# Kernel tuning notes

Hardware: AMD Instinct MI355X
Metric: run time of the kernel (lower is better)

The kernel has to match this reference:

```python
import jax, jax.numpy as jnp
import numpy as np

B, C, H, W = 4, 64, 64, 64  # prompt and kv share the same BCHW shape
EPS = 1e-5
OFR = 4.0  # offset_range_factor
SCALE = (C // 1) ** -0.5  # n_head_channels = dim / n_heads = 64


def conv1x1(x, w, b=None):
    y = jnp.einsum('oc,bchw->bohw', w, x)
    if b is not None:
        y = y + b[None, :, None, None]
    return y


def grid_sample_bilinear(img, grid):
    # img: [N,C,Hp,Wp], grid: [N,Hg,Wg,2] with (x,y) in [-1,1], align_corners=True, zeros padding
    N, Cc, Hp, Wp = img.shape
    Hg, Wg = grid.shape[1], grid.shape[2]
    gx = (grid[..., 0] + 1.0) * 0.5 * (Wp - 1)
    gy = (grid[..., 1] + 1.0) * 0.5 * (Hp - 1)
    x0 = jnp.floor(gx)
    y0 = jnp.floor(gy)
    img_f = img.reshape(N, Cc, Hp * Wp)

    def gather(xi, yi):
        valid = (xi >= 0) & (xi <= Wp - 1) & (yi >= 0) & (yi <= Hp - 1)
        xi_c = jnp.clip(xi, 0, Wp - 1).astype(jnp.int32)
        yi_c = jnp.clip(yi, 0, Hp - 1).astype(jnp.int32)
        idx = (yi_c * Wp + xi_c).reshape(N, 1, -1)
        vals = jnp.take_along_axis(img_f, idx, axis=2)  # [N,C,Hg*Wg]
        return vals, valid.reshape(N, 1, -1).astype(img.dtype)

    v00, m00 = gather(x0, y0)
    v01, m01 = gather(x0 + 1, y0)
    v10, m10 = gather(x0, y0 + 1)
    v11, m11 = gather(x0 + 1, y0 + 1)
    wx = (gx - x0).reshape(N, 1, -1)
    wy = (gy - y0).reshape(N, 1, -1)
    out = (v00 * m00 * (1 - wx) * (1 - wy) + v01 * m01 * wx * (1 - wy)
           + v10 * m10 * (1 - wx) * wy + v11 * m11 * wx * wy)
    return out.reshape(N, Cc, Hg, Wg)


def setup_inputs() -> dict:
    key = jax.random.key(0)
    ks = jax.random.split(key, 8)
    s = 0.02
    return {
        'prompt': jax.random.normal(ks[0], (B, C, H, W), jnp.float32),
        'kv': jax.random.normal(ks[1], (B, C, H, W), jnp.float32),
        'wq': s * jax.random.normal(ks[2], (C, C), jnp.float32),
        'bq': jnp.zeros((C,), jnp.float32),
        'wk': s * jax.random.normal(ks[3], (C, C), jnp.float32),
        'bk': jnp.zeros((C,), jnp.float32),
        'wv': s * jax.random.normal(ks[4], (C, C), jnp.float32),
        'bv': jnp.zeros((C,), jnp.float32),
        'wo': s * jax.random.normal(ks[5], (C, C), jnp.float32),
        'bo': jnp.zeros((C,), jnp.float32),
        'dw_w': s * jax.random.normal(ks[6], (C, 1, 3, 3), jnp.float32),  # depthwise 3x3
        'dw_b': jnp.zeros((C,), jnp.float32),
        'ln_w': jnp.ones((C,), jnp.float32),
        'ln_b': jnp.zeros((C,), jnp.float32),
        'off_w': s * jax.random.normal(ks[7], (2, C), jnp.float32),  # 1x1 conv to 2 offset channels
    }


def reference(prompt, kv, wq, bq, wk, bk, wv, bv, wo, bo, dw_w, dw_b, ln_w, ln_b, off_w):
    # q projection (n_groups=1 so group view == full view)
    q = conv1x1(prompt, wq, bq)  # [B,C,H,W]

    # conv_offset: depthwise 3x3 -> WithBias LayerNorm over channels -> GELU -> 1x1 to 2ch
    t = jax.lax.conv_general_dilated(q, dw_w, (1, 1), ((1, 1), (1, 1)),
                                     feature_group_count=C)
    t = t + dw_b[None, :, None, None]
    mu = t.mean(axis=1, keepdims=True)
    var = t.var(axis=1, keepdims=True)
    t = (t - mu) / jnp.sqrt(var + EPS) * ln_w[None, :, None, None] + ln_b[None, :, None, None]
    t = jax.nn.gelu(t, approximate=False)
    offset = jnp.einsum('oc,bchw->bohw', off_w, t)  # [B,2,H,W] (y,x) channels

    Hk, Wk = offset.shape[2], offset.shape[3]
    n = Hk * Wk
    rng = jnp.array([1.0 / (Hk - 1.0), 1.0 / (Wk - 1.0)], dtype=offset.dtype).reshape(1, 2, 1, 1)
    offset = jnp.tanh(offset) * rng * OFR
    offset = jnp.transpose(offset, (0, 2, 3, 1))  # [B,Hk,Wk,2] (y,x)

    ref_y = (jnp.linspace(0.5, Hk - 0.5, Hk) / (Hk - 1.0)) * 2.0 - 1.0
    ref_x = (jnp.linspace(0.5, Wk - 0.5, Wk) / (Wk - 1.0)) * 2.0 - 1.0
    ry, rx = jnp.meshgrid(ref_y, ref_x, indexing='ij')
    ref = jnp.stack((ry, rx), axis=-1)[None].astype(offset.dtype)  # [1,Hk,Wk,2]

    pos = offset + ref
    grid = pos[..., ::-1]  # swap to (x,y)
    xs = grid_sample_bilinear(kv, grid)  # [B,C,Hk,Wk]
    xs = xs.reshape(B, C, n)

    k = jnp.einsum('oc,bcn->bon', wk, xs) + bk[None, :, None]
    v = jnp.einsum('oc,bcn->bon', wv, xs) + bv[None, :, None]
    qf = q.reshape(B, C, H * W)

    attn = jnp.einsum('bcm,bcn->bmn', qf, k) * SCALE  # [B,HW,n]
    attn = jax.nn.softmax(attn, axis=2)
    out = jnp.einsum('bmn,bcn->bcm', attn, v).reshape(B, C, H, W)
    return conv1x1(out, wo, bo)
```

## Files before the change

### kernel.cpp

```cpp
#include <hip/hip_runtime.h>
#include <math.h>

#define BB 4
#define CC 64
#define HH 64
#define WW 64
#define HWP 4096
#define NPTS 4096
#define NSPLIT 2
#define LDP 72
constexpr float K_EPS   = 1e-5f;
constexpr float K_SCALE = 0.125f;
constexpr float K_OFR   = 4.0f;

#define QF_OFF  0
#define QB_OFF  1048576
#define GXY_OFF 1572864
#define KB_OFF  1605632
#define VB_OFF  2129920
#define OP_OFF  2654208
#define DP_OFF  4751360

typedef short frag8 __attribute__((ext_vector_type(8)));
typedef float f32x4 __attribute__((ext_vector_type(4)));

static __device__ inline unsigned short f2bf(float f) {
  unsigned int u = __builtin_bit_cast(unsigned int, f);
  unsigned int r = (u + 0x7fffu + ((u >> 16) & 1u)) >> 16;
  return (unsigned short)r;
}

__global__ __launch_bounds__(256) void k_qproj(
    const float* __restrict__ prompt, const float* __restrict__ wq,
    const float* __restrict__ bq, float* __restrict__ qf,
    unsigned short* __restrict__ qb) {
  __shared__ float w_s[64 * 64];
  __shared__ float p_s[64 * 64];
  __shared__ unsigned short t_s[64 * 68];
  int tid = threadIdx.x;
  int blk = blockIdx.x;
  int b = blk >> 6; int hw0 = (blk & 63) * 64;
#pragma unroll
  for (int i = 0; i < 16; ++i) w_s[i * 256 + tid] = wq[i * 256 + tid];
#pragma unroll
  for (int i = 0; i < 16; ++i) {
    int idx = i * 256 + tid; int c = idx >> 6, pix = idx & 63;
    p_s[idx] = prompt[(size_t)(b * CC + c) * HWP + hw0 + pix];
  }
  __syncthreads();
  int x = tid & 63, og = tid >> 6;
  float acc[16];
#pragma unroll
  for (int oo = 0; oo < 16; ++oo) acc[oo] = bq[og * 16 + oo];
  for (int cg = 0; cg < 16; ++cg) {
    float p0 = p_s[(cg * 4 + 0) * 64 + x];
    float p1 = p_s[(cg * 4 + 1) * 64 + x];
    float p2 = p_s[(cg * 4 + 2) * 64 + x];
    float p3 = p_s[(cg * 4 + 3) * 64 + x];
#pragma unroll
    for (int oo = 0; oo < 16; ++oo) {
      const float4 w4 = *(const float4*)&w_s[(og * 16 + oo) * 64 + cg * 4];
      acc[oo] = fmaf(w4.x, p0, fmaf(w4.y, p1, fmaf(w4.z, p2, fmaf(w4.w, p3, acc[oo]))));
    }
  }
#pragma unroll
  for (int oo = 0; oo < 16; ++oo) {
    int o = og * 16 + oo;
    qf[(size_t)(b * CC + o) * HWP + hw0 + x] = acc[oo];
    t_s[x * 68 + o] = f2bf(acc[oo]);
  }
  __syncthreads();
#pragma unroll
  for (int i = 0; i < 4; ++i) {
    int idx = i * 256 + tid;
    int pix = idx >> 4, c4 = idx & 15;
    ushort4 v = *(const ushort4*)&t_s[pix * 68 + c4 * 4];
    *(ushort4*)&qb[(size_t)(b * HWP + hw0 + pix) * CC + c4 * 4] = v;
  }
}

__global__ __launch_bounds__(256) void k_offsets(
    const float* __restrict__ q, const float* __restrict__ dw_w,
    const float* __restrict__ dw_b, const float* __restrict__ ln_w,
    const float* __restrict__ ln_b, const float* __restrict__ off_w,
    float* __restrict__ gxy) {
  int tid = threadIdx.x;
  int x = tid & 63;
  int cg = tid >> 6;
  int by = blockIdx.x;
  int b = by >> 6;
  int y = by & 63;

  __shared__ float red0[4][64];
  __shared__ float red1[4][64];

  float t[16];
#pragma unroll
  for (int i = 0; i < 16; ++i) {
    int c = cg * 16 + i;
    float acc = dw_b[c];
    const float* qc = q + (size_t)(b * CC + c) * HWP;
#pragma unroll
    for (int ky = 0; ky < 3; ++ky) {
      int yy = y + ky - 1;
      bool yok = (yy >= 0) && (yy < HH);
#pragma unroll
      for (int kx = 0; kx < 3; ++kx) {
        int xx = x + kx - 1;
        bool ok = yok && (xx >= 0) && (xx < WW);
        float v = ok ? qc[yy * WW + xx] : 0.f;
        acc = fmaf(dw_w[c * 9 + ky * 3 + kx], v, acc);
      }
    }
    t[i] = acc;
  }
  float s1 = 0.f, s2 = 0.f;
#pragma unroll
  for (int i = 0; i < 16; ++i) { s1 += t[i]; s2 += t[i] * t[i]; }
  red0[cg][x] = s1;
  red1[cg][x] = s2;
  __syncthreads();
  float mu = (red0[0][x] + red0[1][x] + red0[2][x] + red0[3][x]) * (1.f / 64.f);
  float ms = (red1[0][x] + red1[1][x] + red1[2][x] + red1[3][x]) * (1.f / 64.f);
  float rstd = rsqrtf(ms - mu * mu + K_EPS);

  float oy = 0.f, ox = 0.f;
#pragma unroll
  for (int i = 0; i < 16; ++i) {
    int c = cg * 16 + i;
    float g = (t[i] - mu) * rstd * ln_w[c] + ln_b[c];
    g = 0.5f * g * (1.f + erff(g * 0.70710678118654752f));
    oy = fmaf(off_w[c], g, oy);
    ox = fmaf(off_w[CC + c], g, ox);
  }
  __syncthreads();
  red0[cg][x] = oy;
  red1[cg][x] = ox;
  __syncthreads();
  if (cg == 0) {
    float osy = red0[0][x] + red0[1][x] + red0[2][x] + red0[3][x];
    float osx = red1[0][x] + red1[1][x] + red1[2][x] + red1[3][x];
    osy = tanhf(osy) * (K_OFR / (HH - 1));
    osx = tanhf(osx) * (K_OFR / (WW - 1));
    float ry = (y + 0.5f) * (2.f / 63.f) - 1.f;
    float rx = (x + 0.5f) * (2.f / 63.f) - 1.f;
    float gx = (osx + rx + 1.f) * 0.5f * (WW - 1);
    float gy = (osy + ry + 1.f) * 0.5f * (HH - 1);
    int n = y * WW + x;
    gxy[(b * HWP + n) * 2 + 0] = gx;
    gxy[(b * HWP + n) * 2 + 1] = gy;
  }
}

__global__ __launch_bounds__(256) void k_sample_kv(
    const float* __restrict__ kv, const float* __restrict__ gxy,
    const float* __restrict__ wk, const float* __restrict__ bk,
    const float* __restrict__ wv, const float* __restrict__ bv,
    unsigned short* __restrict__ kb, unsigned short* __restrict__ vb) {
  __shared__ float wk_s[64 * 64];
  __shared__ float wv_s[64 * 64];
  __shared__ float xs_s[64 * 64];
  int tid = threadIdx.x;
  int blk = blockIdx.x;
  int b = blk >> 6; int n0 = (blk & 63) * 64;
#pragma unroll
  for (int i = 0; i < 16; ++i) {
    wk_s[i * 256 + tid] = wk[i * 256 + tid];
    wv_s[i * 256 + tid] = wv[i * 256 + tid];
  }
  int n = tid & 63, og = tid >> 6;
  int p = b * HWP + n0 + n;
  float gx = gxy[p * 2 + 0], gy = gxy[p * 2 + 1];
  float x0f = floorf(gx), y0f = floorf(gy);
  float wx = gx - x0f, wy = gy - y0f;
  int x0 = (int)x0f, y0 = (int)y0f;
  int x1 = x0 + 1, y1 = y0 + 1;
  float m00 = (x0 >= 0 && x0 < WW && y0 >= 0 && y0 < HH) ? 1.f : 0.f;
  float m01 = (x1 >= 0 && x1 < WW && y0 >= 0 && y0 < HH) ? 1.f : 0.f;
  float m10 = (x0 >= 0 && x0 < WW && y1 >= 0 && y1 < HH) ? 1.f : 0.f;
  float m11 = (x1 >= 0 && x1 < WW && y1 >= 0 && y1 < HH) ? 1.f : 0.f;
  int x0c = min(max(x0, 0), WW - 1), x1c = min(max(x1, 0), WW - 1);
  int y0c = min(max(y0, 0), HH - 1), y1c = min(max(y1, 0), HH - 1);
  int i00 = y0c * WW + x0c, i01 = y0c * WW + x1c;
  int i10 = y1c * WW + x0c, i11 = y1c * WW + x1c;
  float w00 = m00 * (1.f - wx) * (1.f - wy);
  float w01 = m01 * wx * (1.f - wy);
  float w10 = m10 * (1.f - wx) * wy;
  float w11 = m11 * wx * wy;

  const float* base = kv + (size_t)b * CC * HWP;
#pragma unroll 4
  for (int i = 0; i < 16; ++i) {
    int c = og * 16 + i;
    const float* pc = base + (size_t)c * HWP;
    xs_s[c * 64 + n] = w00 * pc[i00] + w01 * pc[i01] + w10 * pc[i10] + w11 * pc[i11];
  }
  __syncthreads();
  float ak[16], av[16];
#pragma unroll
  for (int oo = 0; oo < 16; ++oo) { ak[oo] = bk[og * 16 + oo]; av[oo] = bv[og * 16 + oo]; }
  for (int cg = 0; cg < 16; ++cg) {
    float p0 = xs_s[(cg * 4 + 0) * 64 + n];
    float p1 = xs_s[(cg * 4 + 1) * 64 + n];
    float p2 = xs_s[(cg * 4 + 2) * 64 + n];
    float p3 = xs_s[(cg * 4 + 3) * 64 + n];
#pragma unroll
    for (int oo = 0; oo < 16; ++oo) {
      int o = og * 16 + oo;
      const float4 k4 = *(const float4*)&wk_s[o * 64 + cg * 4];
      const float4 v4 = *(const float4*)&wv_s[o * 64 + cg * 4];
      ak[oo] = fmaf(k4.x, p0, fmaf(k4.y, p1, fmaf(k4.z, p2, fmaf(k4.w, p3, ak[oo]))));
      av[oo] = fmaf(v4.x, p0, fmaf(v4.y, p1, fmaf(v4.z, p2, fmaf(v4.w, p3, av[oo]))));
    }
  }
  unsigned short tk[16];
#pragma unroll
  for (int oo = 0; oo < 16; ++oo) tk[oo] = f2bf(ak[oo]);
  size_t krow = (size_t)(b * NPTS + n0 + n) * CC + og * 16;
  *(uint4*)&kb[krow]     = *(const uint4*)&tk[0];
  *(uint4*)&kb[krow + 8] = *(const uint4*)&tk[8];
#pragma unroll
  for (int oo = 0; oo < 16; ++oo) {
    int o = og * 16 + oo;
    vb[(size_t)(b * CC + o) * NPTS + n0 + n] = f2bf(av[oo]);
  }
}

__global__ __launch_bounds__(256) void k_attn(
    const unsigned short* __restrict__ qb, const unsigned short* __restrict__ kb,
    const unsigned short* __restrict__ vb, float* __restrict__ opart,
    float* __restrict__ dpart) {
  __shared__ short q_s[64 * LDP];
  __shared__ short k_s[64 * LDP];
  __shared__ short v_s[64 * LDP];
  __shared__ short p_s[64 * LDP];

  int tid = threadIdx.x;
  int w = tid >> 6, lane = tid & 63, quad = lane >> 4, l16 = lane & 15;
  int blk = blockIdx.x;
  int mt = blk & 63; int bns = blk >> 6; int ns = bns & 1; int b = bns >> 1;
  int m0 = mt * 64;

  const unsigned short* qbb = qb + (size_t)b * HWP * CC;
  const unsigned short* kbb = kb + (size_t)b * NPTS * CC;
  const unsigned short* vbb = vb + (size_t)b * CC * NPTS;

#pragma unroll
  for (int pass = 0; pass < 2; ++pass) {
    int idx = pass * 256 + tid;
    int row = idx >> 3, part = idx & 7;
    uint4 d = *(const uint4*)(qbb + (size_t)(m0 + row) * CC + part * 8);
    *(uint4*)&q_s[row * LDP + part * 8] = d;
  }

  f32x4 o_acc[4];
  float d_acc[4];
#pragma unroll
  for (int i = 0; i < 4; ++i) {
    d_acc[i] = 0.f;
    o_acc[i][0] = 0.f; o_acc[i][1] = 0.f; o_acc[i][2] = 0.f; o_acc[i][3] = 0.f;
  }

  int nbase = ns * (NPTS / NSPLIT);
  for (int it = 0; it < (NPTS / NSPLIT) / 64; ++it) {
    int n0 = nbase + it * 64;
    __syncthreads();
#pragma unroll
    for (int pass = 0; pass < 2; ++pass) {
      int idx = pass * 256 + tid;
      int row = idx >> 3, part = idx & 7;
      uint4 dk = *(const uint4*)(kbb + (size_t)(n0 + row) * CC + part * 8);
      uint4 dv = *(const uint4*)(vbb + (size_t)row * NPTS + n0 + part * 8);
      *(uint4*)&k_s[row * LDP + part * 8] = dk;
      *(uint4*)&v_s[row * LDP + part * 8] = dv;
    }
    __syncthreads();

    f32x4 s_acc[4];
#pragma unroll
    for (int t = 0; t < 4; ++t) {
      s_acc[t][0] = 0.f; s_acc[t][1] = 0.f; s_acc[t][2] = 0.f; s_acc[t][3] = 0.f;
    }
#pragma unroll
    for (int kc = 0; kc < 2; ++kc) {
      frag8 a = *(const frag8*)&q_s[(w * 16 + l16) * LDP + kc * 32 + quad * 8];
#pragma unroll
      for (int t = 0; t < 4; ++t) {
        frag8 bf = *(const frag8*)&k_s[(t * 16 + l16) * LDP + kc * 32 + quad * 8];
        s_acc[t] = __builtin_amdgcn_mfma_f32_16x16x32_bf16(a, bf, s_acc[t], 0, 0, 0);
      }
    }
#pragma unroll
    for (int t = 0; t < 4; ++t) {
#pragma unroll
      for (int r = 0; r < 4; ++r) {
        float pv = __expf(s_acc[t][r] * K_SCALE);
        unsigned short ph = f2bf(pv);
        p_s[(w * 16 + quad * 4 + r) * LDP + t * 16 + l16] = (short)ph;
        d_acc[r] += __builtin_bit_cast(float, (unsigned int)ph << 16);
      }
    }
#pragma unroll
    for (int kc = 0; kc < 2; ++kc) {
      frag8 bp = *(const frag8*)&p_s[(w * 16 + l16) * LDP + kc * 32 + quad * 8];
#pragma unroll
      for (int ct = 0; ct < 4; ++ct) {
        frag8 av = *(const frag8*)&v_s[(ct * 16 + l16) * LDP + kc * 32 + quad * 8];
        o_acc[ct] = __builtin_amdgcn_mfma_f32_16x16x32_bf16(av, bp, o_acc[ct], 0, 0, 0);
      }
    }
  }

  float* op = opart + (size_t)(ns * BB + b) * HWP * CC + (size_t)(m0 + w * 16 + l16) * CC;
#pragma unroll
  for (int ct = 0; ct < 4; ++ct) {
    float4 o4;
    o4.x = o_acc[ct][0]; o4.y = o_acc[ct][1]; o4.z = o_acc[ct][2]; o4.w = o_acc[ct][3];
    *(float4*)&op[ct * 16 + quad * 4] = o4;
  }
#pragma unroll
  for (int r = 0; r < 4; ++r) {
    float d = d_acc[r];
    d += __shfl_xor(d, 1); d += __shfl_xor(d, 2);
    d += __shfl_xor(d, 4); d += __shfl_xor(d, 8);
    if (l16 == 0)
      dpart[(ns * BB + b) * HWP + m0 + w * 16 + quad * 4 + r] = d;
  }
}

__global__ __launch_bounds__(256) void k_out(
    const float* __restrict__ opart, const float* __restrict__ dpart,
    const float* __restrict__ wo, const float* __restrict__ bo,
    float* __restrict__ out) {
  __shared__ float wo_s[CC * CC];
  __shared__ float t_s[64 * 65];
  int tid = threadIdx.x;
  int blk = blockIdx.x;
  int b = blk >> 6, mt = blk & 63, m0 = mt * 64;
  for (int i = tid; i < CC * CC; i += 256) wo_s[i] = wo[i];

  const float* o0 = opart + (size_t)(0 * BB + b) * HWP * CC;
  const float* o1 = opart + (size_t)(1 * BB + b) * HWP * CC;
  const float* d0 = dpart + (0 * BB + b) * HWP;
  const float* d1 = dpart + (1 * BB + b) * HWP;
#pragma unroll
  for (int it = 0; it < 16; ++it) {
    int idx = it * 256 + tid;
    int m = idx >> 6, c = idx & 63;
    float denom = d0[m0 + m] + d1[m0 + m];
    float val = (o0[(size_t)(m0 + m) * CC + c] + o1[(size_t)(m0 + m) * CC + c]) / denom;
    t_s[m * 65 + c] = val;
  }
  __syncthreads();
  int ml = tid & 63, og = tid >> 6;
  for (int oo = 0; oo < 16; ++oo) {
    int o = og * 16 + oo;
    float acc = bo[o];
#pragma unroll
    for (int c = 0; c < 64; ++c) acc = fmaf(wo_s[o * CC + c], t_s[ml * 65 + c], acc);
    out[(size_t)(b * CC + o) * HWP + m0 + ml] = acc;
  }
}

extern "C" void kernel_launch(void* const* d_in, const int* in_sizes, int n_in,
                              void* d_out, int out_size, void* d_ws, size_t ws_size,
                              hipStream_t stream) {
  const float* prompt = (const float*)d_in[0];
  const float* kv     = (const float*)d_in[1];
  const float* wq     = (const float*)d_in[2];
  const float* bq     = (const float*)d_in[3];
  const float* wk     = (const float*)d_in[4];
  const float* bk     = (const float*)d_in[5];
  const float* wv     = (const float*)d_in[6];
  const float* bv     = (const float*)d_in[7];
  const float* wo     = (const float*)d_in[8];
  const float* bo     = (const float*)d_in[9];
  const float* dw_w   = (const float*)d_in[10];
  const float* dw_b   = (const float*)d_in[11];
  const float* ln_w   = (const float*)d_in[12];
  const float* ln_b   = (const float*)d_in[13];
  const float* off_w  = (const float*)d_in[14];
  float* out = (float*)d_out;
  float* ws  = (float*)d_ws;

  float* qf             = ws + QF_OFF;
  unsigned short* qb    = (unsigned short*)(ws + QB_OFF);
  float* gxy            = ws + GXY_OFF;
  unsigned short* kb    = (unsigned short*)(ws + KB_OFF);
  unsigned short* vb    = (unsigned short*)(ws + VB_OFF);
  float* opart          = ws + OP_OFF;
  float* dpart          = ws + DP_OFF;

  hipLaunchKernelGGL(k_qproj, dim3(BB * 64), dim3(256), 0, stream,
                     prompt, wq, bq, qf, qb);
  hipLaunchKernelGGL(k_offsets, dim3(BB * HH), dim3(256), 0, stream,
                     qf, dw_w, dw_b, ln_w, ln_b, off_w, gxy);
  hipLaunchKernelGGL(k_sample_kv, dim3(BB * 64), dim3(256), 0, stream,
                     kv, gxy, wk, bk, wv, bv, kb, vb);
  hipLaunchKernelGGL(k_attn, dim3(BB * NSPLIT * 64), dim3(256), 0, stream,
                     qb, kb, vb, opart, dpart);
  hipLaunchKernelGGL(k_out, dim3(BB * 64), dim3(256), 0, stream,
                     opart, dpart, wo, bo, out);
}
```

Baseline: 182.5 us.

## Split attention over four key chunks with atomic accumulation and widen prep kernels

Attention blocks now split the key dimension into four chunks instead of two. Partial outputs and denominators are accumulated with atomics into one buffer that is zeroed by a memset, so k_out reads a single partial. The softmax scale is folded into the bf16 Q, Q fragments are held in registers, and the Q and P shared buffers are merged. The projection, offset and sampling kernels run 512 threads with half the per-thread work. More atomic traffic and an extra memset are traded for more blocks and a smaller reduction in the output kernel.

```diff
diff --git a/kernel.cpp b/kernel.cpp
--- a/kernel.cpp
+++ b/kernel.cpp
@@ -7,10 +7,9 @@
 #define WW 64
 #define HWP 4096
 #define NPTS 4096
-#define NSPLIT 2
+#define NSPLIT 4
 #define LDP 72
 constexpr float K_EPS   = 1e-5f;
-constexpr float K_SCALE = 0.125f;
 constexpr float K_OFR   = 4.0f;
 
 #define QF_OFF  0
@@ -19,7 +18,7 @@
 #define KB_OFF  1605632
 #define VB_OFF  2129920
 #define OP_OFF  2654208
-#define DP_OFF  4751360
+#define DP_OFF  3702784
 
 typedef short frag8 __attribute__((ext_vector_type(8)));
 typedef float f32x4 __attribute__((ext_vector_type(4)));
@@ -30,7 +29,7 @@
   return (unsigned short)r;
 }
 
-__global__ __launch_bounds__(256) void k_qproj(
+__global__ __launch_bounds__(512) void k_qproj(
     const float* __restrict__ prompt, const float* __restrict__ wq,
     const float* __restrict__ bq, float* __restrict__ qf,
     unsigned short* __restrict__ qb) {
@@ -41,45 +40,45 @@
   int blk = blockIdx.x;
   int b = blk >> 6; int hw0 = (blk & 63) * 64;
 #pragma unroll
-  for (int i = 0; i < 16; ++i) w_s[i * 256 + tid] = wq[i * 256 + tid];
-#pragma unroll
-  for (int i = 0; i < 16; ++i) {
-    int idx = i * 256 + tid; int c = idx >> 6, pix = idx & 63;
+  for (int i = 0; i < 8; ++i) w_s[i * 512 + tid] = wq[i * 512 + tid];
+#pragma unroll
+  for (int i = 0; i < 8; ++i) {
+    int idx = i * 512 + tid; int c = idx >> 6, pix = idx & 63;
     p_s[idx] = prompt[(size_t)(b * CC + c) * HWP + hw0 + pix];
   }
   __syncthreads();
   int x = tid & 63, og = tid >> 6;
-  float acc[16];
-#pragma unroll
-  for (int oo = 0; oo < 16; ++oo) acc[oo] = bq[og * 16 + oo];
+  float acc[8];
+#pragma unroll
+  for (int oo = 0; oo < 8; ++oo) acc[oo] = bq[og * 8 + oo];
   for (int cg = 0; cg < 16; ++cg) {
     float p0 = p_s[(cg * 4 + 0) * 64 + x];
     float p1 = p_s[(cg * 4 + 1) * 64 + x];
     float p2 = p_s[(cg * 4 + 2) * 64 + x];
     float p3 = p_s[(cg * 4 + 3) * 64 + x];
 #pragma unroll
-    for (int oo = 0; oo < 16; ++oo) {
-      const float4 w4 = *(const float4*)&w_s[(og * 16 + oo) * 64 + cg * 4];
+    for (int oo = 0; oo < 8; ++oo) {
+      const float4 w4 = *(const float4*)&w_s[(og * 8 + oo) * 64 + cg * 4];
       acc[oo] = fmaf(w4.x, p0, fmaf(w4.y, p1, fmaf(w4.z, p2, fmaf(w4.w, p3, acc[oo]))));
     }
   }
 #pragma unroll
-  for (int oo = 0; oo < 16; ++oo) {
-    int o = og * 16 + oo;
+  for (int oo = 0; oo < 8; ++oo) {
+    int o = og * 8 + oo;
     qf[(size_t)(b * CC + o) * HWP + hw0 + x] = acc[oo];
-    t_s[x * 68 + o] = f2bf(acc[oo]);
-  }
-  __syncthreads();
-#pragma unroll
-  for (int i = 0; i < 4; ++i) {
-    int idx = i * 256 + tid;
+    t_s[x * 68 + o] = f2bf(acc[oo] * 0.125f);
+  }
+  __syncthreads();
+#pragma unroll
+  for (int i = 0; i < 2; ++i) {
+    int idx = i * 512 + tid;
     int pix = idx >> 4, c4 = idx & 15;
     ushort4 v = *(const ushort4*)&t_s[pix * 68 + c4 * 4];
     *(ushort4*)&qb[(size_t)(b * HWP + hw0 + pix) * CC + c4 * 4] = v;
   }
 }
 
-__global__ __launch_bounds__(256) void k_offsets(
+__global__ __launch_bounds__(512) void k_offsets(
     const float* __restrict__ q, const float* __restrict__ dw_w,
     const float* __restrict__ dw_b, const float* __restrict__ ln_w,
     const float* __restrict__ ln_b, const float* __restrict__ off_w,
@@ -91,13 +90,13 @@
   int b = by >> 6;
   int y = by & 63;
 
-  __shared__ float red0[4][64];
-  __shared__ float red1[4][64];
-
-  float t[16];
-#pragma unroll
-  for (int i = 0; i < 16; ++i) {
-    int c = cg * 16 + i;
+  __shared__ float red0[8][64];
+  __shared__ float red1[8][64];
+
+  float t[8];
+#pragma unroll
+  for (int i = 0; i < 8; ++i) {
+    int c = cg * 8 + i;
     float acc = dw_b[c];
     const float* qc = q + (size_t)(b * CC + c) * HWP;
 #pragma unroll
@@ -116,18 +115,20 @@
   }
   float s1 = 0.f, s2 = 0.f;
 #pragma unroll
-  for (int i = 0; i < 16; ++i) { s1 += t[i]; s2 += t[i] * t[i]; }
+  for (int i = 0; i < 8; ++i) { s1 += t[i]; s2 += t[i] * t[i]; }
   red0[cg][x] = s1;
   red1[cg][x] = s2;
   __syncthreads();
-  float mu = (red0[0][x] + red0[1][x] + red0[2][x] + red0[3][x]) * (1.f / 64.f);
-  float ms = (red1[0][x] + red1[1][x] + red1[2][x] + red1[3][x]) * (1.f / 64.f);
+  float mu = 0.f, ms = 0.f;
+#pragma unroll
+  for (int g = 0; g < 8; ++g) { mu += red0[g][x]; ms += red1[g][x]; }
+  mu *= (1.f / 64.f); ms *= (1.f / 64.f);
   float rstd = rsqrtf(ms - mu * mu + K_EPS);
 
   float oy = 0.f, ox = 0.f;
 #pragma unroll
-  for (int i = 0; i < 16; ++i) {
-    int c = cg * 16 + i;
+  for (int i = 0; i < 8; ++i) {
+    int c = cg * 8 + i;
     float g = (t[i] - mu) * rstd * ln_w[c] + ln_b[c];
     g = 0.5f * g * (1.f + erff(g * 0.70710678118654752f));
     oy = fmaf(off_w[c], g, oy);
@@ -138,8 +139,9 @@
   red1[cg][x] = ox;
   __syncthreads();
   if (cg == 0) {
-    float osy = red0[0][x] + red0[1][x] + red0[2][x] + red0[3][x];
-    float osx = red1[0][x] + red1[1][x] + red1[2][x] + red1[3][x];
+    float osy = 0.f, osx = 0.f;
+#pragma unroll
+    for (int g = 0; g < 8; ++g) { osy += red0[g][x]; osx += red1[g][x]; }
     osy = tanhf(osy) * (K_OFR / (HH - 1));
     osx = tanhf(osx) * (K_OFR / (WW - 1));
     float ry = (y + 0.5f) * (2.f / 63.f) - 1.f;
@@ -152,7 +154,7 @@
   }
 }
 
-__global__ __launch_bounds__(256) void k_sample_kv(
+__global__ __launch_bounds__(512) void k_sample_kv(
     const float* __restrict__ kv, const float* __restrict__ gxy,
     const float* __restrict__ wk, const float* __restrict__ bk,
     const float* __restrict__ wv, const float* __restrict__ bv,
@@ -164,9 +166,9 @@
   int blk = blockIdx.x;
   int b = blk >> 6; int n0 = (blk & 63) * 64;
 #pragma unroll
-  for (int i = 0; i < 16; ++i) {
-    wk_s[i * 256 + tid] = wk[i * 256 + tid];
-    wv_s[i * 256 + tid] = wv[i * 256 + tid];
+  for (int i = 0; i < 8; ++i) {
+    wk_s[i * 512 + tid] = wk[i * 512 + tid];
+    wv_s[i * 512 + tid] = wv[i * 512 + tid];
   }
   int n = tid & 63, og = tid >> 6;
   int p = b * HWP + n0 + n;
@@ -189,39 +191,38 @@
   float w11 = m11 * wx * wy;
 
   const float* base = kv + (size_t)b * CC * HWP;
-#pragma unroll 4
-  for (int i = 0; i < 16; ++i) {
-    int c = og * 16 + i;
+#pragma unroll
+  for (int i = 0; i < 8; ++i) {
+    int c = og * 8 + i;
     const float* pc = base + (size_t)c * HWP;
     xs_s[c * 64 + n] = w00 * pc[i00] + w01 * pc[i01] + w10 * pc[i10] + w11 * pc[i11];
   }
   __syncthreads();
-  float ak[16], av[16];
-#pragma unroll
-  for (int oo = 0; oo < 16; ++oo) { ak[oo] = bk[og * 16 + oo]; av[oo] = bv[og * 16 + oo]; }
+  float ak[8], av[8];
+#pragma unroll
+  for (int oo = 0; oo < 8; ++oo) { ak[oo] = bk[og * 8 + oo]; av[oo] = bv[og * 8 + oo]; }
   for (int cg = 0; cg < 16; ++cg) {
     float p0 = xs_s[(cg * 4 + 0) * 64 + n];
     float p1 = xs_s[(cg * 4 + 1) * 64 + n];
     float p2 = xs_s[(cg * 4 + 2) * 64 + n];
     float p3 = xs_s[(cg * 4 + 3) * 64 + n];
 #pragma unroll
-    for (int oo = 0; oo < 16; ++oo) {
-      int o = og * 16 + oo;
+    for (int oo = 0; oo < 8; ++oo) {
+      int o = og * 8 + oo;
       const float4 k4 = *(const float4*)&wk_s[o * 64 + cg * 4];
       const float4 v4 = *(const float4*)&wv_s[o * 64 + cg * 4];
       ak[oo] = fmaf(k4.x, p0, fmaf(k4.y, p1, fmaf(k4.z, p2, fmaf(k4.w, p3, ak[oo]))));
       av[oo] = fmaf(v4.x, p0, fmaf(v4.y, p1, fmaf(v4.z, p2, fmaf(v4.w, p3, av[oo]))));
     }
   }
-  unsigned short tk[16];
-#pragma unroll
-  for (int oo = 0; oo < 16; ++oo) tk[oo] = f2bf(ak[oo]);
-  size_t krow = (size_t)(b * NPTS + n0 + n) * CC + og * 16;
-  *(uint4*)&kb[krow]     = *(const uint4*)&tk[0];
-  *(uint4*)&kb[krow + 8] = *(const uint4*)&tk[8];
-#pragma unroll
-  for (int oo = 0; oo < 16; ++oo) {
-    int o = og * 16 + oo;
+  unsigned short tk[8];
+#pragma unroll
+  for (int oo = 0; oo < 8; ++oo) tk[oo] = f2bf(ak[oo]);
+  size_t krow = (size_t)(b * NPTS + n0 + n) * CC + og * 8;
+  *(uint4*)&kb[krow] = *(const uint4*)&tk[0];
+#pragma unroll
+  for (int oo = 0; oo < 8; ++oo) {
+    int o = og * 8 + oo;
     vb[(size_t)(b * CC + o) * NPTS + n0 + n] = f2bf(av[oo]);
   }
 }
@@ -230,15 +231,14 @@
     const unsigned short* __restrict__ qb, const unsigned short* __restrict__ kb,
     const unsigned short* __restrict__ vb, float* __restrict__ opart,
     float* __restrict__ dpart) {
-  __shared__ short q_s[64 * LDP];
+  __shared__ short qp_s[64 * LDP];
   __shared__ short k_s[64 * LDP];
   __shared__ short v_s[64 * LDP];
-  __shared__ short p_s[64 * LDP];
 
   int tid = threadIdx.x;
   int w = tid >> 6, lane = tid & 63, quad = lane >> 4, l16 = lane & 15;
   int blk = blockIdx.x;
-  int mt = blk & 63; int bns = blk >> 6; int ns = bns & 1; int b = bns >> 1;
+  int mt = blk & 63; int bns = blk >> 6; int ns = bns & 3; int b = bns >> 2;
   int m0 = mt * 64;
 
   const unsigned short* qbb = qb + (size_t)b * HWP * CC;
@@ -250,8 +250,13 @@
     int idx = pass * 256 + tid;
     int row = idx >> 3, part = idx & 7;
     uint4 d = *(const uint4*)(qbb + (size_t)(m0 + row) * CC + part * 8);
-    *(uint4*)&q_s[row * LDP + part * 8] = d;
-  }
+    *(uint4*)&qp_s[row * LDP + part * 8] = d;
+  }
+  __syncthreads();
+  frag8 a_frag[2];
+#pragma unroll
+  for (int kc = 0; kc < 2; ++kc)
+    a_frag[kc] = *(const frag8*)&qp_s[(w * 16 + l16) * LDP + kc * 32 + quad * 8];
 
   f32x4 o_acc[4];
   float d_acc[4];
@@ -283,26 +288,25 @@
     }
 #pragma unroll
     for (int kc = 0; kc < 2; ++kc) {
-      frag8 a = *(const frag8*)&q_s[(w * 16 + l16) * LDP + kc * 32 + quad * 8];
 #pragma unroll
       for (int t = 0; t < 4; ++t) {
         frag8 bf = *(const frag8*)&k_s[(t * 16 + l16) * LDP + kc * 32 + quad * 8];
-        s_acc[t] = __builtin_amdgcn_mfma_f32_16x16x32_bf16(a, bf, s_acc[t], 0, 0, 0);
+        s_acc[t] = __builtin_amdgcn_mfma_f32_16x16x32_bf16(a_frag[kc], bf, s_acc[t], 0, 0, 0);
       }
     }
 #pragma unroll
     for (int t = 0; t < 4; ++t) {
 #pragma unroll
       for (int r = 0; r < 4; ++r) {
-        float pv = __expf(s_acc[t][r] * K_SCALE);
+        float pv = __expf(s_acc[t][r]);
         unsigned short ph = f2bf(pv);
-        p_s[(w * 16 + quad * 4 + r) * LDP + t * 16 + l16] = (short)ph;
+        qp_s[(w * 16 + quad * 4 + r) * LDP + t * 16 + l16] = (short)ph;
         d_acc[r] += __builtin_bit_cast(float, (unsigned int)ph << 16);
       }
     }
 #pragma unroll
     for (int kc = 0; kc < 2; ++kc) {
-      frag8 bp = *(const frag8*)&p_s[(w * 16 + l16) * LDP + kc * 32 + quad * 8];
+      frag8 bp = *(const frag8*)&qp_s[(w * 16 + l16) * LDP + kc * 32 + quad * 8];
 #pragma unroll
       for (int ct = 0; ct < 4; ++ct) {
         frag8 av = *(const frag8*)&v_s[(ct * 16 + l16) * LDP + kc * 32 + quad * 8];
@@ -311,12 +315,12 @@
     }
   }
 
-  float* op = opart + (size_t)(ns * BB + b) * HWP * CC + (size_t)(m0 + w * 16 + l16) * CC;
+  float* op = opart + (size_t)b * HWP * CC + (size_t)(m0 + w * 16 + l16) * CC;
 #pragma unroll
   for (int ct = 0; ct < 4; ++ct) {
-    float4 o4;
-    o4.x = o_acc[ct][0]; o4.y = o_acc[ct][1]; o4.z = o_acc[ct][2]; o4.w = o_acc[ct][3];
-    *(float4*)&op[ct * 16 + quad * 4] = o4;
+#pragma unroll
+    for (int r = 0; r < 4; ++r)
+      unsafeAtomicAdd(&op[ct * 16 + quad * 4 + r], o_acc[ct][r]);
   }
 #pragma unroll
   for (int r = 0; r < 4; ++r) {
@@ -324,7 +328,7 @@
     d += __shfl_xor(d, 1); d += __shfl_xor(d, 2);
     d += __shfl_xor(d, 4); d += __shfl_xor(d, 8);
     if (l16 == 0)
-      dpart[(ns * BB + b) * HWP + m0 + w * 16 + quad * 4 + r] = d;
+      unsafeAtomicAdd(&dpart[b * HWP + m0 + w * 16 + quad * 4 + r], d);
   }
 }
 
@@ -339,17 +343,14 @@
   int b = blk >> 6, mt = blk & 63, m0 = mt * 64;
   for (int i = tid; i < CC * CC; i += 256) wo_s[i] = wo[i];
 
-  const float* o0 = opart + (size_t)(0 * BB + b) * HWP * CC;
-  const float* o1 = opart + (size_t)(1 * BB + b) * HWP * CC;
-  const float* d0 = dpart + (0 * BB + b) * HWP;
-  const float* d1 = dpart + (1 * BB + b) * HWP;
+  const float* o0 = opart + (size_t)b * HWP * CC;
+  const float* d0 = dpart + b * HWP;
 #pragma unroll
   for (int it = 0; it < 16; ++it) {
     int idx = it * 256 + tid;
     int m = idx >> 6, c = idx & 63;
-    float denom = d0[m0 + m] + d1[m0 + m];
-    float val = (o0[(size_t)(m0 + m) * CC + c] + o1[(size_t)(m0 + m) * CC + c]) / denom;
-    t_s[m * 65 + c] = val;
+    float denom = d0[m0 + m];
+    t_s[m * 65 + c] = o0[(size_t)(m0 + m) * CC + c] / denom;
   }
   __syncthreads();
   int ml = tid & 63, og = tid >> 6;
@@ -391,11 +392,13 @@
   float* opart          = ws + OP_OFF;
   float* dpart          = ws + DP_OFF;
 
-  hipLaunchKernelGGL(k_qproj, dim3(BB * 64), dim3(256), 0, stream,
+  hipMemsetAsync(opart, 0, (size_t)(1048576 + 16384) * sizeof(float), stream);
+
+  hipLaunchKernelGGL(k_qproj, dim3(BB * 64), dim3(512), 0, stream,
                      prompt, wq, bq, qf, qb);
-  hipLaunchKernelGGL(k_offsets, dim3(BB * HH), dim3(256), 0, stream,
+  hipLaunchKernelGGL(k_offsets, dim3(BB * HH), dim3(512), 0, stream,
                      qf, dw_w, dw_b, ln_w, ln_b, off_w, gxy);
-  hipLaunchKernelGGL(k_sample_kv, dim3(BB * 64), dim3(256), 0, stream,
+  hipLaunchKernelGGL(k_sample_kv, dim3(BB * 64), dim3(512), 0, stream,
                      kv, gxy, wk, bk, wv, bv, kb, vb);
   hipLaunchKernelGGL(k_attn, dim3(BB * NSPLIT * 64), dim3(256), 0, stream,
                      qb, kb, vb, opart, dpart);
```

Result: slower. 202.3 us (+10.8%).
